# Optimization experiments

Hardware: AMD Instinct MI355X
Metric: run time of the kernel (lower is better)

Reference implementation:

```python
import jax, jax.numpy as jnp
import numpy as np

B, H, L = 1024, 32, 3
D_S, D_ID = 512, 128
D_STEER = 3 * D_S + D_ID  # 1664
D_HID = 2048
HS, DQ = 16, 64
HDQ = HS * DQ  # 1024


def setup_inputs() -> dict:
    key = jax.random.key(0)
    ks = jax.random.split(key, 18)
    n = lambda k, shape, std: jax.random.normal(k, shape, dtype=jnp.float32) * std
    inp = {
        "x": jax.random.normal(ks[0], (B * H, D_STEER), dtype=jnp.float32),
        "id_in": jax.random.normal(ks[1], (B * H, D_ID), dtype=jnp.float32),
        # per-head content MLP params
        "in_proj_w": n(ks[2], (H, D_STEER, D_S), 0.014),
        "in_proj_b": jnp.zeros((H, D_S), jnp.float32),
        "norm_w": jnp.ones((H, L, D_S), jnp.float32),
        "up_w": n(ks[3], (H, L, D_S, D_HID), 0.014),
        "up_b": jnp.zeros((H, L, D_HID), jnp.float32),
        "down_w": n(ks[4], (H, L, D_HID, D_S), (2.0 / D_HID) ** 0.5),
        "down_b": jnp.zeros((H, L, D_S), jnp.float32),
        # q_proj: Linear(D_steer, 2*HDQ) -> GELU -> Linear(2*HDQ, HDQ)
        "q1_w": n(ks[5], (D_STEER, 2 * HDQ), 0.014),
        "q1_b": jnp.zeros((2 * HDQ,), jnp.float32),
        "q2_w": n(ks[6], (2 * HDQ, HDQ), 0.02),
        "q2_b": jnp.zeros((HDQ,), jnp.float32),
        # k_proj: Linear(D_id, 2*HDQ) -> GELU -> Linear(2*HDQ, HDQ)
        "k1_w": n(ks[7], (D_ID, 2 * HDQ), 0.014),
        "k1_b": jnp.zeros((2 * HDQ,), jnp.float32),
        "k2_w": n(ks[8], (2 * HDQ, HDQ), 0.02),
        "k2_b": jnp.zeros((HDQ,), jnp.float32),
    }
    return inp


def _per_head_mlp(x, in_proj_w, in_proj_b, norm_w, up_w, up_b, down_w, down_b):
    # x: [B*H, D_steer] -> [B*H, D_s]
    bh = x.shape[0]
    b = bh // H
    xh = x.reshape(b, H, D_STEER)
    h = jnp.einsum("bhd,hde->bhe", xh, in_proj_w) + in_proj_b[None]
    for i in range(norm_w.shape[1]):
        rms = jax.lax.rsqrt(jnp.mean(h * h, axis=-1, keepdims=True) + 1e-6)
        xn = h * rms * norm_w[:, i][None]
        hid = jax.nn.gelu(jnp.einsum("bhd,hde->bhe", xn, up_w[:, i]) + up_b[:, i][None], approximate=False)
        h = h + jnp.einsum("bhd,hde->bhe", hid, down_w[:, i]) + down_b[:, i][None]
    return h.reshape(bh, D_S)


def reference(x, id_in, in_proj_w, in_proj_b, norm_w, up_w, up_b, down_w, down_b,
              q1_w, q1_b, q2_w, q2_b, k1_w, k1_b, k2_w, k2_b):
    content = _per_head_mlp(x, in_proj_w, in_proj_b, norm_w, up_w, up_b, down_w, down_b)
    q = jax.nn.gelu(x @ q1_w + q1_b, approximate=False) @ q2_w + q2_b
    k = jax.nn.gelu(id_in @ k1_w + k1_b, approximate=False) @ k2_w + k2_b
    # concat outputs: [B*H, D_s + HDQ + HDQ]
    return jnp.concatenate([content, q, k], axis=-1)
```

## Files before the change

kernel.cpp:

```cpp
#include <hip/hip_runtime.h>
#include <hip/hip_bf16.h>
#include <math.h>

#define HH 32
#define LL 3
#define DS 512
#define DID 128
#define DSTEER 1664
#define DHID 2048
#define HDQ 1024
#define BHROWS 32768

typedef __attribute__((ext_vector_type(8))) short short8;
typedef __attribute__((ext_vector_type(4))) float f32x4;

typedef const __attribute__((address_space(1))) unsigned int* gptr_t;
typedef __attribute__((address_space(3))) unsigned int* lptr_t;

#define BAR() __builtin_amdgcn_s_barrier()
#define SB()  __builtin_amdgcn_sched_barrier(0)
#define VMCNT8() asm volatile("s_waitcnt vmcnt(8)")
#define VMCNT2() asm volatile("s_waitcnt vmcnt(2)")
#define VMCNT0() asm volatile("s_waitcnt vmcnt(0)")

__device__ __forceinline__ unsigned short f2bf(float f) {
  union { float f; unsigned int u; } x; x.f = f;
  unsigned int r = (x.u + 0x7FFFu + ((x.u >> 16) & 1u)) >> 16;
  return (unsigned short)r;
}
__device__ __forceinline__ unsigned int pk2(float a, float b) {
  return (unsigned int)f2bf(a) | ((unsigned int)f2bf(b) << 16);
}
__device__ __forceinline__ float gelu_fast(float v) {
  float u = 0.79788456080286536f * v * fmaf(0.044715f * v, v, 1.0f);
  u = fminf(fmaxf(u, -9.0f), 9.0f);
  float t = __builtin_amdgcn_exp2f(-2.8853900817779268f * u);
  float r = __builtin_amdgcn_rcpf(1.0f + t);
  float th = fmaf(-2.0f * t, r, 1.0f);
  return 0.5f * v * (1.0f + th);
}

__global__ void cvt_bf16_kernel(const float4* __restrict__ in, uint2* __restrict__ out, long n4) {
  long i = (long)blockIdx.x * blockDim.x + threadIdx.x;
  long stride = (long)gridDim.x * blockDim.x;
  for (; i < n4; i += stride) {
    float4 v = in[i];
    uint2 o; o.x = pk2(v.x, v.y); o.y = pk2(v.z, v.w);
    out[i] = o;
  }
}

__global__ void cvt_permute_kernel(const float4* __restrict__ in, uint4* __restrict__ out) {
  const int s = blockIdx.x;
  const int b = s >> 5, h = s & 31;
  const long d = (long)h * 1024 + b;
  const float4* src = in + (long)s * (DSTEER / 4);
  uint4* dst = out + d * (DSTEER / 8);
  int t = threadIdx.x;
  if (t < DSTEER / 8) {
    float4 a = src[2 * t], c = src[2 * t + 1];
    uint4 o;
    o.x = pk2(a.x, a.y); o.y = pk2(a.z, a.w);
    o.z = pk2(c.x, c.y); o.w = pk2(c.z, c.w);
    dst[t] = o;
  }
}

__global__ void transpose_cvt_kernel(const float* __restrict__ in, long long in_bstride,
                                     unsigned short* __restrict__ out, long long out_bstride,
                                     int R, int C) {
  __shared__ float t[64][33];
  const int r0 = blockIdx.y * 32;
  const int c0 = blockIdx.x * 64;
  const float* bin = in + (long long)blockIdx.z * in_bstride;
  unsigned short* bout = out + (long long)blockIdx.z * out_bstride;
  const int tid = threadIdx.x;
  const int col = tid & 63, rr = tid >> 6;
  #pragma unroll
  for (int j = 0; j < 8; j++) {
    int r = j * 4 + rr;
    t[col][r] = bin[(size_t)(r0 + r) * C + c0 + col];
  }
  __syncthreads();
  const int rq = (tid & 7) * 4;
  const int cc = tid >> 3;
  #pragma unroll
  for (int j = 0; j < 2; j++) {
    int c = j * 32 + cc;
    float v0 = t[c][rq], v1 = t[c][rq + 1], v2 = t[c][rq + 2], v3 = t[c][rq + 3];
    uint2 o; o.x = pk2(v0, v1); o.y = pk2(v2, v3);
    *(uint2*)&bout[(size_t)(c0 + c) * R + r0 + rq] = o;
  }
}

__global__ void rms_scale_kernel(const float* __restrict__ h,
                                 const float* __restrict__ norm_w,
                                 unsigned short* __restrict__ xn, int layer) {
  int gw = (int)((blockIdx.x * blockDim.x + threadIdx.x) >> 6);
  int lane = threadIdx.x & 63;
  if (gw >= BHROWS) return;
  int head = gw >> 10;
  const float4* hr = (const float4*)(h + (size_t)gw * DS);
  float4 v0 = hr[lane * 2], v1 = hr[lane * 2 + 1];
  float ss = v0.x*v0.x + v0.y*v0.y + v0.z*v0.z + v0.w*v0.w
           + v1.x*v1.x + v1.y*v1.y + v1.z*v1.z + v1.w*v1.w;
  #pragma unroll
  for (int off = 32; off > 0; off >>= 1) ss += __shfl_xor(ss, off, 64);
  float r = rsqrtf(ss * (1.0f / DS) + 1e-6f);
  const float4* nw = (const float4*)(norm_w + ((size_t)head * LL + layer) * DS);
  float4 w0 = nw[lane * 2], w1 = nw[lane * 2 + 1];
  uint4 o;
  o.x = pk2(v0.x * r * w0.x, v0.y * r * w0.y);
  o.y = pk2(v0.z * r * w0.z, v0.w * r * w0.w);
  o.z = pk2(v1.x * r * w1.x, v1.y * r * w1.y);
  o.w = pk2(v1.z * r * w1.z, v1.w * r * w1.w);
  *(uint4*)(xn + (size_t)gw * DS + (size_t)lane * 8) = o;
}

template<int EPI>
__global__ __launch_bounds__(512, 2)
void gemm256_kernel(const unsigned short* __restrict__ A, long long a_hstride, long long a_rstride,
                    const unsigned short* __restrict__ Bt, long long b_hstride,
                    const float* __restrict__ bias, int bias_hstride,
                    const float* __restrict__ resid, long long r_hstride, long long r_rstride,
                    void* __restrict__ Cv, long long c_hstride, long long c_rstride,
                    int gx, int tph, int K) {
  __shared__ unsigned short lds[2 * 2 * 256 * 64];
  const int tid = threadIdx.x;
  const int lane = tid & 63;
  const int wave = tid >> 6;
  const int wr = wave >> 2, wc = wave & 3;
  const int ntot = gridDim.x;
  int id = blockIdx.x;
  { int cpx = ntot >> 3; id = (id & 7) * cpx + (id >> 3); }
  const int head = id / tph;
  const int rem = id % tph;
  const int tn = rem % gx, tm = rem / gx;

  const int l3 = lane >> 3;
  const int gslot = ((lane & 7) ^ l3) * 8;
  const int mbase = wave * 8 + l3;
  const int nbase = (wave >> 2) * 64 + (wave & 3) * 8 + l3;
  const unsigned short* pA = A + (size_t)head * a_hstride
                               + (size_t)(tm * 256 + mbase) * a_rstride + gslot;
  const unsigned short* pB = Bt + (size_t)head * b_hstride
                               + (size_t)(tn * 256 + nbase) * K + gslot;
  const size_t aBlk = (size_t)64 * a_rstride;

  const int physk0 = ((lane >> 4) ^ (lane & 7)) * 8;
  const int physk1 = ((4 + (lane >> 4)) ^ (lane & 7)) * 8;
  const int aRow = wr * 128 + (lane & 15);
  const int bRow = wc * 32 + (lane & 15);

  auto stageA = [&](unsigned short* dstA, int h, size_t kels) {
    #pragma unroll
    for (int i = 0; i < 2; ++i)
      __builtin_amdgcn_global_load_lds(
          (gptr_t)(pA + (size_t)(i * 2 + h) * aBlk + kels),
          (lptr_t)(dstA + ((i * 2 + h) * 64 + wave * 8) * 64), 16, 0, 0);
  };
  auto stageB = [&](unsigned short* dstB, int h, size_t kels) {
    #pragma unroll
    for (int i = 0; i < 2; ++i)
      __builtin_amdgcn_global_load_lds(
          (gptr_t)(pB + (size_t)(i * 128 + h * 32) * K + kels),
          (lptr_t)(dstB + (h * 128 + i * 64 + wave * 8) * 64), 16, 0, 0);
  };

  f32x4 acc[8][4];
  #pragma unroll
  for (int i = 0; i < 8; ++i)
    #pragma unroll
    for (int j = 0; j < 4; ++j) acc[i][j] = (f32x4){0.f, 0.f, 0.f, 0.f};
  short8 a[4][2], b[4][2];

  const int T = K >> 6;
  stageA(lds, 0, 0);
  stageB(lds + 16384, 0, 0);
  stageB(lds + 16384, 1, 0);
  stageA(lds, 1, 0);
  stageA(lds + 32768, 0, 64);
  stageB(lds + 32768 + 16384, 0, 64);
  stageB(lds + 32768 + 16384, 1, 64);
  VMCNT8();
  SB();
  BAR();

  for (int t = 0; t < T; ++t) {
    unsigned short* rA = lds + (t & 1) * 32768;
    unsigned short* rB = rA + 16384;
    unsigned short* nA = lds + ((t + 1) & 1) * 32768;
    const size_t k1 = (size_t)(t + 1) * 64;
    const size_t k2 = (size_t)(t + 2) * 64;
    const bool m1 = (t + 1 < T), m2 = (t + 2 < T);

    #pragma unroll
    for (int j = 0; j < 2; ++j) {
      b[j][0] = *(const short8*)&rB[(bRow + j * 16) * 64 + physk0];
      b[j][1] = *(const short8*)&rB[(bRow + j * 16) * 64 + physk1];
    }
    #pragma unroll
    for (int i = 0; i < 4; ++i) {
      a[i][0] = *(const short8*)&rA[(aRow + i * 16) * 64 + physk0];
      a[i][1] = *(const short8*)&rA[(aRow + i * 16) * 64 + physk1];
    }
    if (m1) stageA(nA, 1, k1);
    __builtin_amdgcn_s_setprio(1);
    #pragma unroll
    for (int i = 0; i < 4; ++i)
      #pragma unroll
      for (int j = 0; j < 2; ++j) {
        acc[i][j] = __builtin_amdgcn_mfma_f32_16x16x32_bf16(a[i][0], b[j][0], acc[i][j], 0, 0, 0);
        acc[i][j] = __builtin_amdgcn_mfma_f32_16x16x32_bf16(a[i][1], b[j][1], acc[i][j], 0, 0, 0);
      }
    __builtin_amdgcn_s_setprio(0);
    BAR();

    #pragma unroll
    for (int j = 0; j < 2; ++j) {
      b[2 + j][0] = *(const short8*)&rB[(128 + bRow + j * 16) * 64 + physk0];
      b[2 + j][1] = *(const short8*)&rB[(128 + bRow + j * 16) * 64 + physk1];
    }
    __builtin_amdgcn_s_setprio(1);
    #pragma unroll
    for (int i = 0; i < 4; ++i)
      #pragma unroll
      for (int j = 0; j < 2; ++j) {
        acc[i][2 + j] = __builtin_amdgcn_mfma_f32_16x16x32_bf16(a[i][0], b[2 + j][0], acc[i][2 + j], 0, 0, 0);
        acc[i][2 + j] = __builtin_amdgcn_mfma_f32_16x16x32_bf16(a[i][1], b[2 + j][1], acc[i][2 + j], 0, 0, 0);
      }
    __builtin_amdgcn_s_setprio(0);
    if (m1) { VMCNT8(); } else { VMCNT0(); }
    SB();
    BAR();

    #pragma unroll
    for (int i = 0; i < 4; ++i) {
      a[i][0] = *(const short8*)&rA[(aRow + (4 + i) * 16) * 64 + physk0];
      a[i][1] = *(const short8*)&rA[(aRow + (4 + i) * 16) * 64 + physk1];
    }
    if (m2) { stageA(rA, 0, k2); stageB(rB, 0, k2); }
    __builtin_amdgcn_s_setprio(1);
    #pragma unroll
    for (int i = 0; i < 4; ++i)
      #pragma unroll
      for (int j = 0; j < 2; ++j) {
        acc[4 + i][2 + j] = __builtin_amdgcn_mfma_f32_16x16x32_bf16(a[i][0], b[2 + j][0], acc[4 + i][2 + j], 0, 0, 0);
        acc[4 + i][2 + j] = __builtin_amdgcn_mfma_f32_16x16x32_bf16(a[i][1], b[2 + j][1], acc[4 + i][2 + j], 0, 0, 0);
      }
    __builtin_amdgcn_s_setprio(0);
    BAR();

    if (m2) stageB(rB, 1, k2);
    __builtin_amdgcn_s_setprio(1);
    #pragma unroll
    for (int i = 0; i < 4; ++i)
      #pragma unroll
      for (int j = 0; j < 2; ++j) {
        acc[4 + i][j] = __builtin_amdgcn_mfma_f32_16x16x32_bf16(a[i][0], b[j][0], acc[4 + i][j], 0, 0, 0);
        acc[4 + i][j] = __builtin_amdgcn_mfma_f32_16x16x32_bf16(a[i][1], b[j][1], acc[4 + i][j], 0, 0, 0);
      }
    __builtin_amdgcn_s_setprio(0);
    if (m2) { VMCNT8(); } else if (m1) { VMCNT2(); }
    SB();
    BAR();
  }

  const float* bptr = bias + (size_t)head * bias_hstride;
  #pragma unroll
  for (int i = 0; i < 8; ++i) {
    #pragma unroll
    for (int j = 0; j < 4; ++j) {
      #pragma unroll
      for (int r = 0; r < 4; ++r) {
        int rowt = wr * 128 + i * 16 + (lane >> 4) * 4 + r;
        int colt = wc * 64 + j * 16 + (lane & 15);
        int col = tn * 256 + colt;
        size_t row = (size_t)(tm * 256 + rowt);
        size_t cidx = (size_t)head * c_hstride + row * c_rstride + col;
        float v = acc[i][j][r] + bptr[col];
        if (EPI == 1) {
          ((unsigned short*)Cv)[cidx] = f2bf(gelu_fast(v));
        } else if (EPI == 2) {
          v += resid[(size_t)head * r_hstride + row * r_rstride + col];
          ((float*)Cv)[cidx] = v;
        } else {
          ((float*)Cv)[cidx] = v;
        }
      }
    }
  }
}

extern "C" void kernel_launch(void* const* d_in, const int* in_sizes, int n_in,
                              void* d_out, int out_size, void* d_ws, size_t ws_size,
                              hipStream_t stream) {
  const float* x         = (const float*)d_in[0];
  const float* id_in     = (const float*)d_in[1];
  const float* in_proj_w = (const float*)d_in[2];
  const float* in_proj_b = (const float*)d_in[3];
  const float* norm_w    = (const float*)d_in[4];
  const float* up_w      = (const float*)d_in[5];
  const float* up_b      = (const float*)d_in[6];
  const float* down_w    = (const float*)d_in[7];
  const float* down_b    = (const float*)d_in[8];
  const float* q1_w      = (const float*)d_in[9];
  const float* q1_b      = (const float*)d_in[10];
  const float* q2_w      = (const float*)d_in[11];
  const float* q2_b      = (const float*)d_in[12];
  const float* k1_w      = (const float*)d_in[13];
  const float* k1_b      = (const float*)d_in[14];
  const float* k2_w      = (const float*)d_in[15];
  const float* k2_b      = (const float*)d_in[16];
  float* out = (float*)d_out;

  char* ws = (char*)d_ws;
  unsigned short* x_hm  = (unsigned short*)ws; ws += (size_t)BHROWS * DSTEER * 2;
  unsigned short* id_bf = (unsigned short*)ws; ws += (size_t)BHROWS * DID * 2;
  float*          hbuf  = (float*)ws;          ws += (size_t)BHROWS * DS * 4;
  unsigned short* xn    = (unsigned short*)ws; ws += (size_t)BHROWS * DS * 2;
  unsigned short* hid   = (unsigned short*)ws; ws += (size_t)BHROWS * DHID * 2;
  unsigned short* wbuf  = (unsigned short*)ws; ws += (size_t)HH * DHID * DS * 2;

  cvt_permute_kernel<<<BHROWS, 256, 0, stream>>>((const float4*)x, (uint4*)x_hm);
  cvt_bf16_kernel<<<512, 256, 0, stream>>>((const float4*)id_in, (uint2*)id_bf,
                                           (long)BHROWS * DID / 4);

  transpose_cvt_kernel<<<dim3(2 * HDQ / 64, DSTEER / 32, 1), 256, 0, stream>>>(
      q1_w, 0, wbuf, 0, DSTEER, 2 * HDQ);
  gemm256_kernel<1><<<1024, 512, 0, stream>>>(
      x_hm, (long long)1024 * DSTEER, DSTEER, wbuf, 0, q1_b, 0, nullptr, 0, 0,
      hid, (long long)1024 * 2 * HDQ, 2 * HDQ, 8, 32, DSTEER);
  transpose_cvt_kernel<<<dim3(HDQ / 64, 2 * HDQ / 32, 1), 256, 0, stream>>>(
      q2_w, 0, wbuf, 0, 2 * HDQ, HDQ);
  gemm256_kernel<0><<<512, 512, 0, stream>>>(
      hid, (long long)1024 * 2 * HDQ, 2 * HDQ, wbuf, 0, q2_b, 0, nullptr, 0, 0,
      out + 512, 2560, (long long)32 * 2560, 4, 16, 2 * HDQ);

  transpose_cvt_kernel<<<dim3(2 * HDQ / 64, DID / 32, 1), 256, 0, stream>>>(
      k1_w, 0, wbuf, 0, DID, 2 * HDQ);
  gemm256_kernel<1><<<1024, 512, 0, stream>>>(
      id_bf, 0, DID, wbuf, 0, k1_b, 0, nullptr, 0, 0,
      hid, 0, 2 * HDQ, 8, 1024, DID);
  transpose_cvt_kernel<<<dim3(HDQ / 64, 2 * HDQ / 32, 1), 256, 0, stream>>>(
      k2_w, 0, wbuf, 0, 2 * HDQ, HDQ);
  gemm256_kernel<0><<<512, 512, 0, stream>>>(
      hid, 0, 2 * HDQ, wbuf, 0, k2_b, 0, nullptr, 0, 0,
      out + 1536, 0, 2560, 4, 512, 2 * HDQ);

  transpose_cvt_kernel<<<dim3(DS / 64, DSTEER / 32, HH), 256, 0, stream>>>(
      in_proj_w, (long long)DSTEER * DS, wbuf, (long long)DS * DSTEER, DSTEER, DS);
  gemm256_kernel<0><<<256, 512, 0, stream>>>(
      x_hm, (long long)1024 * DSTEER, DSTEER, wbuf, (long long)DS * DSTEER,
      in_proj_b, DS, nullptr, 0, 0,
      hbuf, (long long)1024 * DS, DS, 2, 8, DSTEER);

  for (int i = 0; i < LL; i++) {
    rms_scale_kernel<<<8192, 256, 0, stream>>>(hbuf, norm_w, xn, i);
    transpose_cvt_kernel<<<dim3(DHID / 64, DS / 32, HH), 256, 0, stream>>>(
        up_w + (size_t)i * DS * DHID, (long long)LL * DS * DHID,
        wbuf, (long long)DHID * DS, DS, DHID);
    gemm256_kernel<1><<<1024, 512, 0, stream>>>(
        xn, (long long)1024 * DS, DS, wbuf, (long long)DHID * DS,
        up_b + (size_t)i * DHID, LL * DHID, nullptr, 0, 0,
        hid, (long long)1024 * DHID, DHID, 8, 32, DS);
    transpose_cvt_kernel<<<dim3(DS / 64, DHID / 32, HH), 256, 0, stream>>>(
        down_w + (size_t)i * DHID * DS, (long long)LL * DHID * DS,
        wbuf, (long long)DS * DHID, DHID, DS);
    if (i < 2) {
      gemm256_kernel<2><<<256, 512, 0, stream>>>(
          hid, (long long)1024 * DHID, DHID, wbuf, (long long)DS * DHID,
          down_b + (size_t)i * DS, LL * DS,
          hbuf, (long long)1024 * DS, DS,
          hbuf, (long long)1024 * DS, DS, 2, 8, DHID);
    } else {
      gemm256_kernel<2><<<256, 512, 0, stream>>>(
          hid, (long long)1024 * DHID, DHID, wbuf, (long long)DS * DHID,
          down_b + (size_t)i * DS, LL * DS,
          hbuf, (long long)1024 * DS, DS,
          out, 2560, (long long)32 * 2560, 2, 8, DHID);
    }
  }
}
```

Baseline: 1.547 ms.

## Simplify GEMM main loop to plain double buffering with full-tile prefetch

Replaces the staggered two-stage-ahead prefetch schedule, which used partial vmcnt waits and four barrier phases per K-step, with a simple double buffer. Each iteration now issues the whole next tile's A and B loads at once, computes the current tile in two halves, and waits for all loads with vmcnt(0). This cuts the barrier count and the scheduling complexity per step, but it shortens the prefetch distance, so global-load latency may be less well hidden.

```diff
diff --git a/kernel.cpp b/kernel.cpp
--- a/kernel.cpp
+++ b/kernel.cpp
@@ -19,8 +19,6 @@
 
 #define BAR() __builtin_amdgcn_s_barrier()
 #define SB()  __builtin_amdgcn_sched_barrier(0)
-#define VMCNT8() asm volatile("s_waitcnt vmcnt(8)")
-#define VMCNT2() asm volatile("s_waitcnt vmcnt(2)")
 #define VMCNT0() asm volatile("s_waitcnt vmcnt(0)")
 
 __device__ __forceinline__ unsigned short f2bf(float f) {
@@ -176,13 +174,10 @@
 
   const int T = K >> 6;
   stageA(lds, 0, 0);
+  stageA(lds, 1, 0);
   stageB(lds + 16384, 0, 0);
   stageB(lds + 16384, 1, 0);
-  stageA(lds, 1, 0);
-  stageA(lds + 32768, 0, 64);
-  stageB(lds + 32768 + 16384, 0, 64);
-  stageB(lds + 32768 + 16384, 1, 64);
-  VMCNT8();
+  VMCNT0();
   SB();
   BAR();
 
@@ -190,26 +185,31 @@
     unsigned short* rA = lds + (t & 1) * 32768;
     unsigned short* rB = rA + 16384;
     unsigned short* nA = lds + ((t + 1) & 1) * 32768;
+    unsigned short* nB = nA + 16384;
     const size_t k1 = (size_t)(t + 1) * 64;
-    const size_t k2 = (size_t)(t + 2) * 64;
-    const bool m1 = (t + 1 < T), m2 = (t + 2 < T);
-
-    #pragma unroll
-    for (int j = 0; j < 2; ++j) {
-      b[j][0] = *(const short8*)&rB[(bRow + j * 16) * 64 + physk0];
-      b[j][1] = *(const short8*)&rB[(bRow + j * 16) * 64 + physk1];
+    const bool m1 = (t + 1 < T);
+
+    #pragma unroll
+    for (int j = 0; j < 4; ++j) {
+      b[j][0] = *(const short8*)&rB[((j >> 1) * 128 + bRow + (j & 1) * 16) * 64 + physk0];
+      b[j][1] = *(const short8*)&rB[((j >> 1) * 128 + bRow + (j & 1) * 16) * 64 + physk1];
     }
     #pragma unroll
     for (int i = 0; i < 4; ++i) {
       a[i][0] = *(const short8*)&rA[(aRow + i * 16) * 64 + physk0];
       a[i][1] = *(const short8*)&rA[(aRow + i * 16) * 64 + physk1];
     }
-    if (m1) stageA(nA, 1, k1);
+    if (m1) {
+      stageA(nA, 0, k1);
+      stageA(nA, 1, k1);
+      stageB(nB, 0, k1);
+      stageB(nB, 1, k1);
+    }
     __builtin_amdgcn_s_setprio(1);
     #pragma unroll
     for (int i = 0; i < 4; ++i)
       #pragma unroll
-      for (int j = 0; j < 2; ++j) {
+      for (int j = 0; j < 4; ++j) {
         acc[i][j] = __builtin_amdgcn_mfma_f32_16x16x32_bf16(a[i][0], b[j][0], acc[i][j], 0, 0, 0);
         acc[i][j] = __builtin_amdgcn_mfma_f32_16x16x32_bf16(a[i][1], b[j][1], acc[i][j], 0, 0, 0);
       }
@@ -217,51 +217,20 @@
     BAR();
 
     #pragma unroll
-    for (int j = 0; j < 2; ++j) {
-      b[2 + j][0] = *(const short8*)&rB[(128 + bRow + j * 16) * 64 + physk0];
-      b[2 + j][1] = *(const short8*)&rB[(128 + bRow + j * 16) * 64 + physk1];
-    }
-    __builtin_amdgcn_s_setprio(1);
-    #pragma unroll
-    for (int i = 0; i < 4; ++i)
-      #pragma unroll
-      for (int j = 0; j < 2; ++j) {
-        acc[i][2 + j] = __builtin_amdgcn_mfma_f32_16x16x32_bf16(a[i][0], b[2 + j][0], acc[i][2 + j], 0, 0, 0);
-        acc[i][2 + j] = __builtin_amdgcn_mfma_f32_16x16x32_bf16(a[i][1], b[2 + j][1], acc[i][2 + j], 0, 0, 0);
-      }
-    __builtin_amdgcn_s_setprio(0);
-    if (m1) { VMCNT8(); } else { VMCNT0(); }
-    SB();
-    BAR();
-
-    #pragma unroll
     for (int i = 0; i < 4; ++i) {
       a[i][0] = *(const short8*)&rA[(aRow + (4 + i) * 16) * 64 + physk0];
       a[i][1] = *(const short8*)&rA[(aRow + (4 + i) * 16) * 64 + physk1];
     }
-    if (m2) { stageA(rA, 0, k2); stageB(rB, 0, k2); }
     __builtin_amdgcn_s_setprio(1);
     #pragma unroll
     for (int i = 0; i < 4; ++i)
       #pragma unroll
-      for (int j = 0; j < 2; ++j) {
-        acc[4 + i][2 + j] = __builtin_amdgcn_mfma_f32_16x16x32_bf16(a[i][0], b[2 + j][0], acc[4 + i][2 + j], 0, 0, 0);
-        acc[4 + i][2 + j] = __builtin_amdgcn_mfma_f32_16x16x32_bf16(a[i][1], b[2 + j][1], acc[4 + i][2 + j], 0, 0, 0);
-      }
-    __builtin_amdgcn_s_setprio(0);
-    BAR();
-
-    if (m2) stageB(rB, 1, k2);
-    __builtin_amdgcn_s_setprio(1);
-    #pragma unroll
-    for (int i = 0; i < 4; ++i)
-      #pragma unroll
-      for (int j = 0; j < 2; ++j) {
+      for (int j = 0; j < 4; ++j) {
         acc[4 + i][j] = __builtin_amdgcn_mfma_f32_16x16x32_bf16(a[i][0], b[j][0], acc[4 + i][j], 0, 0, 0);
         acc[4 + i][j] = __builtin_amdgcn_mfma_f32_16x16x32_bf16(a[i][1], b[j][1], acc[4 + i][j], 0, 0, 0);
       }
     __builtin_amdgcn_s_setprio(0);
-    if (m2) { VMCNT8(); } else if (m1) { VMCNT2(); }
+    VMCNT0();
     SB();
     BAR();
   }
```

Result: slower. 1.594 ms (+3.1%).
